# Performance work log

Hardware: AMD Instinct MI355X
Metric: run time of the kernel (lower is better)

Reference implementation:

```python
import jax, jax.numpy as jnp
import numpy as np

B, DIM, H, W = 64, 384, 28, 28
NH, HD, WS, SS = 6, 64, 7, 3
HID = 1536
N = WS * WS
NW = (H // WS) * (W // WS)
SCALE = HD ** -0.25  # qk_scale=None -> head_dim ** -0.25, applied to both q and k
EPS = 1e-5


def _rel_pos_index(ws):
    coords = np.stack(np.meshgrid(np.arange(ws), np.arange(ws), indexing='ij'))  # (2,ws,ws)
    flat = coords.reshape(2, -1)
    rel = (flat[:, :, None] - flat[:, None, :]).transpose(1, 2, 0).copy()  # (N,N,2)
    rel[..., 0] += ws - 1
    rel[..., 1] += ws - 1
    rel[..., 0] *= 2 * ws - 1
    return rel.sum(-1)  # (N,N) int


def _attn_mask(h, w, ws, ss):
    img = np.zeros((h, w))
    cnt = 0
    for hs in (slice(0, -ws), slice(-ws, -ss), slice(-ss, None)):
        for wsl in (slice(0, -ws), slice(-ws, -ss), slice(-ss, None)):
            img[hs, wsl] = cnt
            cnt += 1
    mw = img.reshape(h // ws, ws, w // ws, ws).transpose(0, 2, 1, 3).reshape(-1, ws * ws)  # (nW,N)
    diff = mw[:, None, :] - mw[:, :, None]
    return np.where(diff != 0, -100.0, 0.0).astype(np.float32)  # (nW,N,N)


REL_IDX = jnp.asarray(_rel_pos_index(WS))          # (N,N)
MASK = jnp.asarray(_attn_mask(H, W, WS, SS))       # (NW,N,N)


def _layernorm_bchw(x, w, b):
    mean = jnp.mean(x, axis=1, keepdims=True)
    var = jnp.var(x, axis=1, keepdims=True, ddof=1)  # torch.var_mean is unbiased
    return (x - mean) / jnp.sqrt(var + EPS) * w + b


def setup_inputs() -> dict:
    key = jax.random.key(0)
    ks = jax.random.split(key, 6)
    return {
        'x': jax.random.normal(ks[0], (B, DIM, H, W), jnp.float32),
        'norm1_w': jnp.ones((1, DIM, 1, 1), jnp.float32),
        'norm1_b': jnp.zeros((1, DIM, 1, 1), jnp.float32),
        'qkv_w': jax.random.normal(ks[1], (3 * NH * HD, DIM), jnp.float32) * 0.02,
        'rel_bias_table': jax.random.normal(ks[2], ((2 * WS - 1) ** 2, NH), jnp.float32) * 0.02,
        'proj_w': jax.random.normal(ks[3], (DIM, NH * HD), jnp.float32) * 0.02,
        'norm2_w': jnp.ones((1, DIM, 1, 1), jnp.float32),
        'norm2_b': jnp.zeros((1, DIM, 1, 1), jnp.float32),
        'mlp_w1': jax.random.normal(ks[4], (HID, DIM), jnp.float32) * 0.02,
        'mlp_w3': jax.random.normal(ks[5], (DIM, HID), jnp.float32) * 0.02,
    }


def reference(x, norm1_w, norm1_b, qkv_w, rel_bias_table, proj_w, norm2_w, norm2_b, mlp_w1, mlp_w3):
    b = x.shape[0]
    shortcut = x
    xn = _layernorm_bchw(x, norm1_w, norm1_b)
    xs = jnp.roll(xn, (-SS, -SS), axis=(2, 3))
    # window partition: (B,C,H,W) -> (B*nW, C, WS, WS)
    xw = xs.reshape(b, DIM, H // WS, WS, W // WS, WS).transpose(0, 2, 4, 1, 3, 5).reshape(-1, DIM, WS, WS)
    bw = xw.shape[0]
    # 1x1-conv qkv projection (no bias), then split heads
    qkv = jnp.einsum('oc,bchw->bohw', qkv_w, xw).reshape(bw, 3, NH, HD, N)
    q, k, v = jnp.moveaxis(qkv, 1, 0)  # each (bw, NH, HD, N)
    attn = jnp.einsum('bhdn,bhdm->bhnm', q * SCALE, k * SCALE)  # (bw,NH,N,N)
    bias = rel_bias_table[REL_IDX.reshape(-1)].reshape(N, N, NH).transpose(2, 0, 1)  # (NH,N,N)
    attn = attn + bias[None]
    attn = attn.reshape(b, NW, NH, N, N) + MASK[None, :, None]
    attn = jax.nn.softmax(attn.reshape(bw, NH, N, N), axis=-1)
    out = jnp.einsum('bhnm,bhdm->bhdn', attn, v)  # (bw,NH,HD,N)
    out = out.reshape(bw, NH * HD, WS, WS)
    out = jnp.einsum('oc,bchw->bohw', proj_w, out)
    # window reverse + unshift
    xr = out.reshape(b, H // WS, W // WS, DIM, WS, WS).transpose(0, 3, 1, 4, 2, 5).reshape(b, DIM, H, W)
    xr = jnp.roll(xr, (SS, SS), axis=(2, 3))
    x = shortcut + xr
    # conv MLP (1x1 convs, no bias, exact GELU)
    xn2 = _layernorm_bchw(x, norm2_w, norm2_b)
    h = jax.nn.gelu(jnp.einsum('oc,bchw->bohw', mlp_w1, xn2), approximate=False)
    x = x + jnp.einsum('oc,bchw->bohw', mlp_w3, h)
    return x
```

## Files before the change

kernel.cpp:

```cpp
#include <hip/hip_runtime.h>
#include <hip/hip_bf16.h>


typedef __bf16 bf16x8 __attribute__((ext_vector_type(8)));
typedef __bf16 bf16x4 __attribute__((ext_vector_type(4)));
typedef float  f32x4  __attribute__((ext_vector_type(4)));
typedef float  f32x2  __attribute__((ext_vector_type(2)));
typedef int    i32x4  __attribute__((ext_vector_type(4)));
typedef int    i32x2  __attribute__((ext_vector_type(2)));

#define GAS __attribute__((address_space(1)))
#define LAS __attribute__((address_space(3)))

#if __has_builtin(__builtin_amdgcn_cvt_pk_f32_fp8) && __has_builtin(__builtin_amdgcn_cvt_pk_fp8_f32)
#define HAS_HW_FP8 1
#else
#define HAS_HW_FP8 0
#endif

__device__ __forceinline__ int div7u(int m) { return (m * 37) >> 8; }

#if !HAS_HW_FP8
__device__ __forceinline__ float fp8_dec1(unsigned u) {
  unsigned s = (u >> 7) & 1, e = (u >> 3) & 15, m = u & 7;
  float nrm = __uint_as_float((s << 31) | ((e + 120) << 23) | (m << 20));
  float sub = (s ? -1.f : 1.f) * (float)m * 0.001953125f;
  return e ? nrm : sub;
}
__device__ __forceinline__ unsigned fp8_enc1(float f) {
  f = fminf(fmaxf(f, -448.f), 448.f);
  unsigned u = __float_as_uint(f);
  unsigned s = u >> 31;
  int e8 = (int)((u >> 23) & 255) - 120;
  unsigned m32 = u & 0x7fffff;
  if (e8 <= 0) return s << 7;
  unsigned m = m32 >> 20;
  unsigned rem = m32 & 0xfffff;
  m += (rem > 0x80000u) || (rem == 0x80000u && (m & 1));
  if (m == 8) { m = 0; ++e8; }
  if (e8 > 15 || (e8 == 15 && m == 7)) { e8 = 15; m = 6; }
  return (s << 7) | ((unsigned)e8 << 3) | m;
}
#endif

template <bool HI>
__device__ __forceinline__ f32x2 fp8_cvt2(int w) {
#if HAS_HW_FP8
  return __builtin_amdgcn_cvt_pk_f32_fp8(w, HI);
#else
  unsigned b0 = (w >> (HI ? 16 : 0)) & 255, b1 = (w >> (HI ? 24 : 8)) & 255;
  return (f32x2){fp8_dec1(b0), fp8_dec1(b1)};
#endif
}
template <bool HI>
__device__ __forceinline__ int fp8_pk2(float a, float b, int old) {
#if HAS_HW_FP8
  return __builtin_amdgcn_cvt_pk_fp8_f32(a, b, old, HI);
#else
  unsigned v = fp8_enc1(a) | (fp8_enc1(b) << 8);
  return HI ? (int)(((unsigned)old & 0xffffu) | (v << 16))
            : (int)(((unsigned)old & 0xffff0000u) | v);
#endif
}
__device__ __forceinline__ i32x4 fp8x8_to_bf16x8(i32x2 v) {
  f32x2 a = fp8_cvt2<false>(v[0]), b = fp8_cvt2<true>(v[0]);
  f32x2 c = fp8_cvt2<false>(v[1]), d = fp8_cvt2<true>(v[1]);
  bf16x8 r = {(__bf16)a[0], (__bf16)a[1], (__bf16)b[0], (__bf16)b[1],
              (__bf16)c[0], (__bf16)c[1], (__bf16)d[0], (__bf16)d[1]};
  return __builtin_bit_cast(i32x4, r);
}

__device__ __forceinline__ float gelu_f(float v) {
  float u = v * __builtin_fmaf(0.0356774f, v * v, 0.79788456f);
  float e = __expf(2.f * u);
  float t = 1.f - 2.f * __builtin_amdgcn_rcpf(e + 1.f);
  return 0.5f * v * (1.f + t);
}

__global__ __launch_bounds__(256) void cvt_all_kernel(const float* __restrict__ s0,
                                                      const float* __restrict__ s1,
                                                      const float* __restrict__ s2,
                                                      const float* __restrict__ s3,
                                                      __bf16* __restrict__ d0,
                                                      __bf16* __restrict__ d1,
                                                      __bf16* __restrict__ d2,
                                                      __bf16* __restrict__ d3,
                                                      const float* __restrict__ tbl,
                                                      float* __restrict__ be) {
  int i = blockIdx.x * 256 + threadIdx.x;
  if (i < 442368) { d0[i] = (__bf16)s0[i]; return; }
  i -= 442368;
  if (i < 147456) { d1[i] = (__bf16)s1[i]; return; }
  i -= 147456;
  if (i < 589824) { d2[i] = (__bf16)s2[i]; return; }
  i -= 589824;
  if (i < 589824) { d3[i] = (__bf16)s3[i]; return; }
  i -= 589824;
  if (i < 6 * 64 * 64) {
    int m = i & 63, n = (i >> 6) & 63, h = i >> 12;
    float v = 0.f;
    if (m < 49 && n < 49) {
      int in_ = div7u(n), jn = n - in_ * 7;
      int im  = div7u(m), jm = m - im * 7;
      v = tbl[((in_ - im + 6) * 13 + (jn - jm + 6)) * 6 + h];
    }
    be[i] = v;
  }
}

template <typename TIN>
__global__ __launch_bounds__(256) void ln_t_kernel(const TIN* __restrict__ x,
                                                   const float* __restrict__ gw,
                                                   const float* __restrict__ gb,
                                                   __bf16* __restrict__ out) {
  __shared__ f32x4 ps[16][16], ps2[16][16];
  __shared__ __align__(16) __bf16 tile[64][198];
  const int tid = threadIdx.x;
  const int lane = tid & 63, w = tid >> 6;
  const int gq = lane & 15;
  const int sub = (w << 2) + (lane >> 4);
  const int tok0 = blockIdx.x << 6;
  const int tokg4 = tok0 + (gq << 2);
  const unsigned b = (unsigned)tokg4 / 784u;
  const unsigned p = (unsigned)tokg4 - b * 784u;
  const TIN* xp = x + (size_t)b * 301056u + p;

  f32x4 vals[24];
  f32x4 s4 = {0.f, 0.f, 0.f, 0.f}, s24 = {0.f, 0.f, 0.f, 0.f};
  #pragma unroll
  for (int half = 0; half < 2; ++half)
    #pragma unroll
    for (int k = 0; k < 12; ++k) {
      int c = half * 192 + sub * 12 + k;
      f32x4 v;
      if constexpr (sizeof(TIN) == 4) {
        v = *(const f32x4*)(xp + (size_t)c * 784u);
      } else {
        bf16x4 t = *(const bf16x4*)(xp + (size_t)c * 784u);
        v = (f32x4){(float)t[0], (float)t[1], (float)t[2], (float)t[3]};
      }
      vals[half * 12 + k] = v;
      s4 += v;
      s24 += v * v;
    }
  ps[sub][gq] = s4;
  ps2[sub][gq] = s24;
  __syncthreads();
  f32x4 S = {0.f, 0.f, 0.f, 0.f}, S2 = {0.f, 0.f, 0.f, 0.f};
  #pragma unroll
  for (int i = 0; i < 16; ++i) { S += ps[i][gq]; S2 += ps2[i][gq]; }
  f32x4 mean = S * (1.f / 384.f);
  f32x4 var = (S2 - S * mean) * (1.f / 383.f);
  f32x4 rstd;
  #pragma unroll
  for (int j = 0; j < 4; ++j) rstd[j] = rsqrtf(var[j] + 1e-5f);

  #pragma unroll
  for (int half = 0; half < 2; ++half) {
    if (half) __syncthreads();
    #pragma unroll
    for (int k = 0; k < 12; ++k) {
      int c = half * 192 + sub * 12 + k;
      float wgt = gw[c], bia = gb[c];
      f32x4 v = (vals[half * 12 + k] - mean) * rstd * wgt + bia;
      #pragma unroll
      for (int j = 0; j < 4; ++j)
        tile[(gq << 2) + j][sub * 12 + k] = (__bf16)v[j];
    }
    __syncthreads();
    #pragma unroll
    for (int it = 0; it < 6; ++it) {
      int idx = (it << 8) + tid;
      int row = idx / 24, colc = idx - row * 24;
      bf16x8 vv = *(const bf16x8*)(&tile[row][colc << 3]);
      *(bf16x8*)(out + (size_t)(tok0 + row) * 384 + half * 192 + (colc << 3)) = vv;
    }
  }
}

template <int EPI, int F8>
__global__ __launch_bounds__(256, 3) void gemm_bt(const __bf16* __restrict__ A, int lda,
                                                  const void* __restrict__ BtV, int ldb,
                                                  int K, int My,
                                                  void* __restrict__ outT, int ldo, int ocol,
                                                  void* __restrict__ outR,
                                                  const void* __restrict__ resid,
                                                  int tok_off) {
  constexpr bool B8 = (F8 && EPI >= 2);
  constexpr int esz = B8 ? 1 : 2;
  __shared__ __align__(16) char smem[33792];
  const int tid = threadIdx.x;
  const int lane = tid & 63;
  const int w = tid >> 6;
  const int wr = w >> 1, wc = w & 1;
  const int c = lane & 15, g = lane >> 4;

  const int nwg = gridDim.x;
  const int orig = blockIdx.x;
  const int q = nwg >> 3, r = nwg & 7;
  const int xcd = orig & 7, ii = orig >> 3;
  const int wgid = (xcd < r ? xcd * (q + 1) : r * (q + 1) + (xcd - r) * q) + ii;
  const int bx = wgid / My;
  const int by = wgid - bx * My;
  const int m0 = by << 7;
  const int n0 = bx << 7;

  const __bf16* ap[4];
  const unsigned char* bp[4];
  #pragma unroll
  for (int i = 0; i < 4; ++i) {
    int s = (i << 8) + tid;
    int row = s >> 3;
    int kk = ((s ^ row) & 7) << 3;
    ap[i] = A + (size_t)(m0 + row) * lda + kk;
    bp[i] = (const unsigned char*)BtV + ((size_t)(n0 + row) * ldb + kk) * esz;
  }

  i32x4 sA0, sA1, sA2, sA3;
  i32x4 sB0, sB1, sB2, sB3;
  i32x2 t0, t1, t2, t3;
  auto issue = [&](int k0) {
    sA0 = *(const i32x4*)(ap[0] + k0);
    sA1 = *(const i32x4*)(ap[1] + k0);
    sA2 = *(const i32x4*)(ap[2] + k0);
    sA3 = *(const i32x4*)(ap[3] + k0);
    if constexpr (B8) {
      t0 = *(const i32x2*)(bp[0] + k0);
      t1 = *(const i32x2*)(bp[1] + k0);
      t2 = *(const i32x2*)(bp[2] + k0);
      t3 = *(const i32x2*)(bp[3] + k0);
    } else {
      sB0 = *(const i32x4*)(bp[0] + k0 * 2);
      sB1 = *(const i32x4*)(bp[1] + k0 * 2);
      sB2 = *(const i32x4*)(bp[2] + k0 * 2);
      sB3 = *(const i32x4*)(bp[3] + k0 * 2);
    }
  };
  auto write_lds = [&]() {
    *(i32x4*)(smem +         (((0 << 8) + tid) << 4)) = sA0;
    *(i32x4*)(smem +         (((1 << 8) + tid) << 4)) = sA1;
    *(i32x4*)(smem +         (((2 << 8) + tid) << 4)) = sA2;
    *(i32x4*)(smem +         (((3 << 8) + tid) << 4)) = sA3;
    if constexpr (B8) {
      *(i32x4*)(smem + 16384 + (((0 << 8) + tid) << 4)) = fp8x8_to_bf16x8(t0);
      *(i32x4*)(smem + 16384 + (((1 << 8) + tid) << 4)) = fp8x8_to_bf16x8(t1);
      *(i32x4*)(smem + 16384 + (((2 << 8) + tid) << 4)) = fp8x8_to_bf16x8(t2);
      *(i32x4*)(smem + 16384 + (((3 << 8) + tid) << 4)) = fp8x8_to_bf16x8(t3);
    } else {
      *(i32x4*)(smem + 16384 + (((0 << 8) + tid) << 4)) = sB0;
      *(i32x4*)(smem + 16384 + (((1 << 8) + tid) << 4)) = sB1;
      *(i32x4*)(smem + 16384 + (((2 << 8) + tid) << 4)) = sB2;
      *(i32x4*)(smem + 16384 + (((3 << 8) + tid) << 4)) = sB3;
    }
  };

  f32x4 acc[4][4] = {};
  const int nt = K >> 6;

  issue(0);
  write_lds();
  asm volatile("s_waitcnt lgkmcnt(0)" ::: "memory");
  __builtin_amdgcn_s_barrier();
  __builtin_amdgcn_sched_barrier(0);

  for (int t = 0; t < nt; ++t) {
    if (t + 1 < nt) issue((t + 1) << 6);
    const char* smA = smem;
    const char* smB = smem + 16384;
    #pragma unroll
    for (int ks = 0; ks < 2; ++ks) {
      bf16x8 af[4], bfv[4];
      #pragma unroll
      for (int mi = 0; mi < 4; ++mi) {
        int r2 = (wr << 6) + (mi << 4) + c;
        af[mi] = *(const bf16x8*)(smA + (r2 << 7) + (((ks << 6) + (g << 4)) ^ ((r2 & 7) << 4)));
      }
      #pragma unroll
      for (int nj = 0; nj < 4; ++nj) {
        int r2 = (wc << 6) + (nj << 4) + c;
        bfv[nj] = *(const bf16x8*)(smB + (r2 << 7) + (((ks << 6) + (g << 4)) ^ ((r2 & 7) << 4)));
      }
      #pragma unroll
      for (int mi = 0; mi < 4; ++mi)
        #pragma unroll
        for (int nj = 0; nj < 4; ++nj) {
          if constexpr (EPI >= 2)
            acc[mi][nj] = __builtin_amdgcn_mfma_f32_16x16x32_bf16(bfv[nj], af[mi], acc[mi][nj], 0, 0, 0);
          else
            acc[mi][nj] = __builtin_amdgcn_mfma_f32_16x16x32_bf16(af[mi], bfv[nj], acc[mi][nj], 0, 0, 0);
        }
    }
    __builtin_amdgcn_s_barrier();
    if (t + 1 < nt) {
      write_lds();
      asm volatile("s_waitcnt lgkmcnt(0)" ::: "memory");
    }
    __builtin_amdgcn_s_barrier();
    __builtin_amdgcn_sched_barrier(0);
  }

  if constexpr (EPI <= 1) {
    #pragma unroll
    for (int mi = 0; mi < 4; ++mi)
      #pragma unroll
      for (int nj = 0; nj < 4; ++nj) {
        f32x4 v = acc[mi][nj];
        if constexpr (EPI == 1) {
          #pragma unroll
          for (int r2 = 0; r2 < 4; ++r2) v[r2] = gelu_f(v[r2]);
        }
        bf16x4 pk = {(__bf16)v[0], (__bf16)v[1], (__bf16)v[2], (__bf16)v[3]};
        int nl = (wc << 6) + (nj << 4) + c;
        int ml = (wr << 6) + (mi << 4) + (g << 2);
        *(bf16x4*)(smem + nl * 264 + ml * 2) = pk;
      }
    __syncthreads();
    #pragma unroll
    for (int it = 0; it < 8; ++it) {
      int id = (it << 8) + tid;
      int n = id >> 4, mc = id & 15;
      bf16x8 v = *(const bf16x8*)(smem + n * 264 + (mc << 4));
      if constexpr (F8) {
        int w0 = 0, w1 = 0;
        w0 = fp8_pk2<false>((float)v[0], (float)v[1], w0);
        w0 = fp8_pk2<true>((float)v[2], (float)v[3], w0);
        w1 = fp8_pk2<false>((float)v[4], (float)v[5], w1);
        w1 = fp8_pk2<true>((float)v[6], (float)v[7], w1);
        *(i32x2*)((unsigned char*)outT + (size_t)(n0 + n) * ldo + (ocol + m0 + (mc << 3))) =
            (i32x2){w0, w1};
      } else {
        *(bf16x8*)((__bf16*)outT + (size_t)(n0 + n) * ldo + (ocol + m0 + (mc << 3))) = v;
      }
    }
  } else {
    #pragma unroll
    for (int nj = 0; nj < 4; ++nj) {
      int tokb = tok_off + n0 + (wc << 6) + (nj << 4) + (g << 2);
      unsigned bb = (unsigned)tokb / 784u;
      unsigned pp = (unsigned)tokb - bb * 784u;
      size_t base2 = (size_t)bb * (384u * 784u) + pp;
      #pragma unroll
      for (int mi = 0; mi < 4; ++mi) {
        int o = m0 + (wr << 6) + (mi << 4) + c;
        size_t a2 = base2 + (size_t)o * 784u;
        if constexpr (EPI == 2) {
          bf16x4 rv = *(const bf16x4*)((const __bf16*)resid + a2);
          f32x4 v;
          #pragma unroll
          for (int j = 0; j < 4; ++j) v[j] = acc[mi][nj][j] + (float)rv[j];
          *(f32x4*)((float*)outR + a2) = v;
        } else {
          f32x4 rv = *(const f32x4*)((const float*)resid + a2);
          f32x4 v = acc[mi][nj] + rv;
          bf16x4 pk = {(__bf16)v[0], (__bf16)v[1], (__bf16)v[2], (__bf16)v[3]};
          *(bf16x4*)((__bf16*)outR + a2) = pk;
        }
      }
    }
  }
}

__global__ __launch_bounds__(256, 2) void attn_kernel(const __bf16* __restrict__ qkv,
                                                      const float* __restrict__ be,
                                                      __bf16* __restrict__ outt) {
  __shared__ __align__(16) char smem_all[4][16384];
  const int tid = threadIdx.x;
  const int lane = tid & 63;
  const int w = tid >> 6;
  char* sm = (char*)smem_all[w];
  const int pair = blockIdx.x * 4 + w;
  const int h = pair % 6;
  const int wg = pair / 6;
  const int b = wg >> 4;
  const int wi = wg & 15;
  const int wh = wi >> 2, wwi = wi & 3;
  const int cc = lane & 15, g = lane >> 4;

  {
    int rsub = lane >> 3;
    int slot = lane & 7;
    int dc = (slot ^ rsub) << 3;
    #pragma unroll
    for (int i = 0; i < 8; ++i) {
      int r = i * 8 + rsub;
      int m = r < 49 ? r : 48;
      int im = div7u(m), jm = m - im * 7;
      int sh = wh * 7 + im + 3; if (sh >= 28) sh -= 28;
      int sw = wwi * 7 + jm + 3; if (sw >= 28) sw -= 28;
      size_t trow = (size_t)(b * 784 + sh * 28 + sw) * 1152;
      __builtin_amdgcn_global_load_lds((const GAS void*)(qkv + trow + 384 + h * 64 + dc),
                                       (LAS void*)(sm + i * 1024), 16, 0, 0);
      __builtin_amdgcn_global_load_lds((const GAS void*)(qkv + trow + h * 64 + dc),
                                       (LAS void*)(sm + 8192 + i * 1024), 16, 0, 0);
    }
  }
  asm volatile("s_waitcnt vmcnt(0)" ::: "memory");
  __syncthreads();

  f32x4 sacc[4][4] = {};
  #pragma unroll
  for (int ks = 0; ks < 2; ++ks) {
    bf16x8 kf[4], qf[4];
    #pragma unroll
    for (int mi = 0; mi < 4; ++mi) {
      int r = (mi << 4) + cc;
      kf[mi] = *(const bf16x8*)(sm + (r << 7) + (((ks << 6) + (g << 4)) ^ ((r & 7) << 4)));
    }
    #pragma unroll
    for (int nj = 0; nj < 4; ++nj) {
      int r = (nj << 4) + cc;
      qf[nj] = *(const bf16x8*)(sm + 8192 + (r << 7) + (((ks << 6) + (g << 4)) ^ ((r & 7) << 4)));
    }
    #pragma unroll
    for (int mi = 0; mi < 4; ++mi)
      #pragma unroll
      for (int nj = 0; nj < 4; ++nj)
        sacc[mi][nj] = __builtin_amdgcn_mfma_f32_16x16x32_bf16(kf[mi], qf[nj], sacc[mi][nj], 0, 0, 0);
  }
  __syncthreads();

  int r9m[4][4];
  #pragma unroll
  for (int mi = 0; mi < 4; ++mi)
    #pragma unroll
    for (int rr = 0; rr < 4; ++rr) {
      int m = (mi << 4) + (g << 2) + rr; if (m > 48) m = 48;
      int im = div7u(m), jm = m - im * 7;
      int sh = wh * 7 + im, sw = wwi * 7 + jm;
      r9m[mi][rr] = ((sh < 21) ? 0 : (sh < 25 ? 1 : 2)) * 3 + ((sw < 21) ? 0 : (sw < 25 ? 1 : 2));
    }

  #pragma unroll
  for (int nj = 0; nj < 4; ++nj) {
    int n = (nj << 4) + cc;
    int ncl = n > 48 ? 48 : n;
    int in_ = div7u(ncl), jn = ncl - in_ * 7;
    int shn = wh * 7 + in_, swn = wwi * 7 + jn;
    int r9n = ((shn < 21) ? 0 : (shn < 25 ? 1 : 2)) * 3 + ((swn < 21) ? 0 : (swn < 25 ? 1 : 2));
    float mx = -1e30f;
    #pragma unroll
    for (int mi = 0; mi < 4; ++mi) {
      f32x4 bia = *(const f32x4*)(be + (((h << 6) + n) << 6) + (mi << 4) + (g << 2));
      #pragma unroll
      for (int rr = 0; rr < 4; ++rr) {
        int m = (mi << 4) + (g << 2) + rr;
        float t = (m < 49)
            ? sacc[mi][nj][rr] * 0.125f + bia[rr] + ((r9m[mi][rr] == r9n) ? 0.f : -100.f)
            : -1e30f;
        sacc[mi][nj][rr] = t;
        mx = fmaxf(mx, t);
      }
    }
    mx = fmaxf(mx, __shfl_xor(mx, 16, 64));
    mx = fmaxf(mx, __shfl_xor(mx, 32, 64));
    float sum = 0.f;
    #pragma unroll
    for (int mi = 0; mi < 4; ++mi)
      #pragma unroll
      for (int rr = 0; rr < 4; ++rr) {
        float e = __expf(sacc[mi][nj][rr] - mx);
        sacc[mi][nj][rr] = e;
        sum += e;
      }
    sum += __shfl_xor(sum, 16, 64);
    sum += __shfl_xor(sum, 32, 64);
    float inv = __builtin_amdgcn_rcpf(sum);
    #pragma unroll
    for (int mi = 0; mi < 4; ++mi) {
      bf16x4 pk = {(__bf16)(sacc[mi][nj][0] * inv), (__bf16)(sacc[mi][nj][1] * inv),
                   (__bf16)(sacc[mi][nj][2] * inv), (__bf16)(sacc[mi][nj][3] * inv)};
      *(bf16x4*)(sm + 8192 + (n << 7) + (((mi << 5) + (g << 3)) ^ ((n & 7) << 4))) = pk;
    }
  }

  {
    int ml = lane & 15, dq = lane >> 4;
    #pragma unroll
    for (int it = 0; it < 4; ++it) {
      int m = (it << 4) + ml;
      int mc_ = m > 48 ? 48 : m;
      int im = div7u(mc_), jm = mc_ - im * 7;
      int sh = wh * 7 + im + 3; if (sh >= 28) sh -= 28;
      int sw = wwi * 7 + jm + 3; if (sw >= 28) sw -= 28;
      const __bf16* gv = qkv + (size_t)(b * 784 + sh * 28 + sw) * 1152 + 768 + h * 64;
      #pragma unroll
      for (int hd = 0; hd < 2; ++hd) {
        int dbase = (hd << 5) + (dq << 3);
        bf16x8 v = *(const bf16x8*)(gv + dbase);
        #pragma unroll
        for (int j = 0; j < 8; ++j) {
          int d = dbase + j;
          *(__bf16*)(sm + (d << 7) + ((((m >> 3) ^ (d & 7)) << 4) + ((m & 7) << 1))) = v[j];
        }
      }
    }
  }
  __syncthreads();

  f32x4 oacc[4][4] = {};
  #pragma unroll
  for (int ks = 0; ks < 2; ++ks) {
    bf16x8 pf[4], vf[4];
    #pragma unroll
    for (int ni = 0; ni < 4; ++ni) {
      int n = (ni << 4) + cc;
      pf[ni] = *(const bf16x8*)(sm + 8192 + (n << 7) + (((ks << 6) + (g << 4)) ^ ((n & 7) << 4)));
    }
    #pragma unroll
    for (int dj = 0; dj < 4; ++dj) {
      int d = (dj << 4) + cc;
      vf[dj] = *(const bf16x8*)(sm + (d << 7) + ((((ks << 2) + g) ^ (d & 7)) << 4));
    }
    #pragma unroll
    for (int ni = 0; ni < 4; ++ni)
      #pragma unroll
      for (int dj = 0; dj < 4; ++dj)
        oacc[ni][dj] = __builtin_amdgcn_mfma_f32_16x16x32_bf16(pf[ni], vf[dj], oacc[ni][dj], 0, 0, 0);
  }

  #pragma unroll
  for (int ni = 0; ni < 4; ++ni)
    #pragma unroll
    for (int rr = 0; rr < 4; ++rr) {
      int n = (ni << 4) + (g << 2) + rr;
      if (n < 49) {
        int im = div7u(n), jn = n - im * 7;
        int sh = wh * 7 + im + 3; if (sh >= 28) sh -= 28;
        int sw = wwi * 7 + jn + 3; if (sw >= 28) sw -= 28;
        __bf16* op = outt + (size_t)(b * 784 + sh * 28 + sw) * 384 + h * 64;
        #pragma unroll
        for (int dj = 0; dj < 4; ++dj)
          op[(dj << 4) + cc] = (__bf16)oacc[ni][dj][rr];
      }
    }
}

extern "C" void kernel_launch(void* const* d_in, const int* in_sizes, int n_in,
                              void* d_out, int out_size, void* d_ws, size_t ws_size,
                              hipStream_t stream) {
  (void)in_sizes; (void)n_in; (void)out_size; (void)ws_size;
  const float* x     = (const float*)d_in[0];
  const float* n1w   = (const float*)d_in[1];
  const float* n1b   = (const float*)d_in[2];
  const float* qkvw  = (const float*)d_in[3];
  const float* tbl   = (const float*)d_in[4];
  const float* projw = (const float*)d_in[5];
  const float* n2w   = (const float*)d_in[6];
  const float* n2b   = (const float*)d_in[7];
  const float* w1    = (const float*)d_in[8];
  const float* w3    = (const float*)d_in[9];
  float* out = (float*)d_out;

  char* ws = (char*)d_ws;
  __bf16* bufA = (__bf16*)ws;
  unsigned char* h8 = (unsigned char*)(ws + 38535168);
  __bf16* x2b = (__bf16*)(ws + 38535168 + 77070336);
  float*  be   = (float*)(ws + 154140672);
  __bf16* wq   = (__bf16*)(ws + 154238976);
  __bf16* wp   = wq + 442368;
  __bf16* wm1  = wp + 147456;
  __bf16* wm3  = wm1 + 589824;

  cvt_all_kernel<<<7008, 256, 0, stream>>>(qkvw, projw, w1, w3, wq, wp, wm1, wm3, tbl, be);

  ln_t_kernel<float><<<784, 256, 0, stream>>>(x, n1w, n1b, bufA);
  gemm_bt<0, 0><<<392 * 9, 256, 0, stream>>>(wq, 384, bufA, 384, 384, 9,
                                             (void*)h8, 1152, 0, nullptr, nullptr, 0);
  attn_kernel<<<1536, 256, 0, stream>>>((const __bf16*)h8, be, bufA);
  gemm_bt<3, 0><<<392 * 3, 256, 0, stream>>>(wp, 384, bufA, 384, 384, 3,
                                             nullptr, 0, 0, (void*)x2b, x, 0);
  ln_t_kernel<__bf16><<<784, 256, 0, stream>>>(x2b, n2w, n2b, bufA);
  gemm_bt<1, 1><<<392 * 12, 256, 0, stream>>>(wm1, 384, bufA, 384, 384, 12,
                                              (void*)h8, 1536, 0, nullptr, nullptr, 0);
  gemm_bt<2, 1><<<392 * 3, 256, 0, stream>>>(wm3, 1536, (const void*)h8, 1536, 1536, 3,
                                             nullptr, 0, 0, out, x2b, 0);
}
```

Measured before the change: 344.8 us.

## Run MLP down-projection as native FP8 MFMA GEMM with scaled FP8 weights

Converts the w3 weight to FP8 with a scale of 8 and adds a dedicated gemm_f8 kernel that feeds FP8 operands straight into fp8 MFMA instructions. The old path converted FP8 activations to bf16 in registers before the LDS write. The new path halves the LDS footprint, drops the unpack work and allows higher occupancy. The cost is extra precision loss from quantising the weights to FP8, and the fused residual epilogue is duplicated in a new kernel.

```diff
diff --git a/kernel.cpp b/kernel.cpp
--- a/kernel.cpp
+++ b/kernel.cpp
@@ -5,14 +5,13 @@
 typedef __bf16 bf16x8 __attribute__((ext_vector_type(8)));
 typedef __bf16 bf16x4 __attribute__((ext_vector_type(4)));
 typedef float  f32x4  __attribute__((ext_vector_type(4)));
-typedef float  f32x2  __attribute__((ext_vector_type(2)));
 typedef int    i32x4  __attribute__((ext_vector_type(4)));
 typedef int    i32x2  __attribute__((ext_vector_type(2)));
 
 #define GAS __attribute__((address_space(1)))
 #define LAS __attribute__((address_space(3)))
 
-#if __has_builtin(__builtin_amdgcn_cvt_pk_f32_fp8) && __has_builtin(__builtin_amdgcn_cvt_pk_fp8_f32)
+#if __has_builtin(__builtin_amdgcn_cvt_pk_fp8_f32)
 #define HAS_HW_FP8 1
 #else
 #define HAS_HW_FP8 0
@@ -21,12 +20,6 @@
 __device__ __forceinline__ int div7u(int m) { return (m * 37) >> 8; }
 
 #if !HAS_HW_FP8
-__device__ __forceinline__ float fp8_dec1(unsigned u) {
-  unsigned s = (u >> 7) & 1, e = (u >> 3) & 15, m = u & 7;
-  float nrm = __uint_as_float((s << 31) | ((e + 120) << 23) | (m << 20));
-  float sub = (s ? -1.f : 1.f) * (float)m * 0.001953125f;
-  return e ? nrm : sub;
-}
 __device__ __forceinline__ unsigned fp8_enc1(float f) {
   f = fminf(fmaxf(f, -448.f), 448.f);
   unsigned u = __float_as_uint(f);
@@ -44,15 +37,6 @@
 #endif
 
 template <bool HI>
-__device__ __forceinline__ f32x2 fp8_cvt2(int w) {
-#if HAS_HW_FP8
-  return __builtin_amdgcn_cvt_pk_f32_fp8(w, HI);
-#else
-  unsigned b0 = (w >> (HI ? 16 : 0)) & 255, b1 = (w >> (HI ? 24 : 8)) & 255;
-  return (f32x2){fp8_dec1(b0), fp8_dec1(b1)};
-#endif
-}
-template <bool HI>
 __device__ __forceinline__ int fp8_pk2(float a, float b, int old) {
 #if HAS_HW_FP8
   return __builtin_amdgcn_cvt_pk_fp8_f32(a, b, old, HI);
@@ -62,13 +46,6 @@
             : (int)(((unsigned)old & 0xffff0000u) | v);
 #endif
 }
-__device__ __forceinline__ i32x4 fp8x8_to_bf16x8(i32x2 v) {
-  f32x2 a = fp8_cvt2<false>(v[0]), b = fp8_cvt2<true>(v[0]);
-  f32x2 c = fp8_cvt2<false>(v[1]), d = fp8_cvt2<true>(v[1]);
-  bf16x8 r = {(__bf16)a[0], (__bf16)a[1], (__bf16)b[0], (__bf16)b[1],
-              (__bf16)c[0], (__bf16)c[1], (__bf16)d[0], (__bf16)d[1]};
-  return __builtin_bit_cast(i32x4, r);
-}
 
 __device__ __forceinline__ float gelu_f(float v) {
   float u = v * __builtin_fmaf(0.0356774f, v * v, 0.79788456f);
@@ -84,7 +61,7 @@
                                                       __bf16* __restrict__ d0,
                                                       __bf16* __restrict__ d1,
                                                       __bf16* __restrict__ d2,
-                                                      __bf16* __restrict__ d3,
+                                                      unsigned char* __restrict__ d3,
                                                       const float* __restrict__ tbl,
                                                       float* __restrict__ be) {
   int i = blockIdx.x * 256 + threadIdx.x;
@@ -94,8 +71,13 @@
   i -= 147456;
   if (i < 589824) { d2[i] = (__bf16)s2[i]; return; }
   i -= 589824;
-  if (i < 589824) { d3[i] = (__bf16)s3[i]; return; }
-  i -= 589824;
+  if (i < 294912) {
+    int j = i << 1;
+    int v = fp8_pk2<false>(s3[j] * 8.f, s3[j + 1] * 8.f, 0);
+    ((unsigned short*)d3)[i] = (unsigned short)((unsigned)v & 0xffffu);
+    return;
+  }
+  i -= 294912;
   if (i < 6 * 64 * 64) {
     int m = i & 63, n = (i >> 6) & 63, h = i >> 12;
     float v = 0.f;
@@ -180,14 +162,11 @@
 
 template <int EPI, int F8>
 __global__ __launch_bounds__(256, 3) void gemm_bt(const __bf16* __restrict__ A, int lda,
-                                                  const void* __restrict__ BtV, int ldb,
+                                                  const __bf16* __restrict__ Bt, int ldb,
                                                   int K, int My,
                                                   void* __restrict__ outT, int ldo, int ocol,
                                                   void* __restrict__ outR,
-                                                  const void* __restrict__ resid,
-                                                  int tok_off) {
-  constexpr bool B8 = (F8 && EPI >= 2);
-  constexpr int esz = B8 ? 1 : 2;
+                                                  const float* __restrict__ resid) {
   __shared__ __align__(16) char smem[33792];
   const int tid = threadIdx.x;
   const int lane = tid & 63;
@@ -206,52 +185,36 @@
   const int n0 = bx << 7;
 
   const __bf16* ap[4];
-  const unsigned char* bp[4];
+  const __bf16* bp[4];
   #pragma unroll
   for (int i = 0; i < 4; ++i) {
     int s = (i << 8) + tid;
     int row = s >> 3;
     int kk = ((s ^ row) & 7) << 3;
     ap[i] = A + (size_t)(m0 + row) * lda + kk;
-    bp[i] = (const unsigned char*)BtV + ((size_t)(n0 + row) * ldb + kk) * esz;
-  }
-
-  i32x4 sA0, sA1, sA2, sA3;
-  i32x4 sB0, sB1, sB2, sB3;
-  i32x2 t0, t1, t2, t3;
+    bp[i] = Bt + (size_t)(n0 + row) * ldb + kk;
+  }
+
+  i32x4 sA0, sA1, sA2, sA3, sB0, sB1, sB2, sB3;
   auto issue = [&](int k0) {
     sA0 = *(const i32x4*)(ap[0] + k0);
     sA1 = *(const i32x4*)(ap[1] + k0);
     sA2 = *(const i32x4*)(ap[2] + k0);
     sA3 = *(const i32x4*)(ap[3] + k0);
-    if constexpr (B8) {
-      t0 = *(const i32x2*)(bp[0] + k0);
-      t1 = *(const i32x2*)(bp[1] + k0);
-      t2 = *(const i32x2*)(bp[2] + k0);
-      t3 = *(const i32x2*)(bp[3] + k0);
-    } else {
-      sB0 = *(const i32x4*)(bp[0] + k0 * 2);
-      sB1 = *(const i32x4*)(bp[1] + k0 * 2);
-      sB2 = *(const i32x4*)(bp[2] + k0 * 2);
-      sB3 = *(const i32x4*)(bp[3] + k0 * 2);
-    }
+    sB0 = *(const i32x4*)(bp[0] + k0);
+    sB1 = *(const i32x4*)(bp[1] + k0);
+    sB2 = *(const i32x4*)(bp[2] + k0);
+    sB3 = *(const i32x4*)(bp[3] + k0);
   };
   auto write_lds = [&]() {
     *(i32x4*)(smem +         (((0 << 8) + tid) << 4)) = sA0;
     *(i32x4*)(smem +         (((1 << 8) + tid) << 4)) = sA1;
     *(i32x4*)(smem +         (((2 << 8) + tid) << 4)) = sA2;
     *(i32x4*)(smem +         (((3 << 8) + tid) << 4)) = sA3;
-    if constexpr (B8) {
-      *(i32x4*)(smem + 16384 + (((0 << 8) + tid) << 4)) = fp8x8_to_bf16x8(t0);
-      *(i32x4*)(smem + 16384 + (((1 << 8) + tid) << 4)) = fp8x8_to_bf16x8(t1);
-      *(i32x4*)(smem + 16384 + (((2 << 8) + tid) << 4)) = fp8x8_to_bf16x8(t2);
-      *(i32x4*)(smem + 16384 + (((3 << 8) + tid) << 4)) = fp8x8_to_bf16x8(t3);
-    } else {
-      *(i32x4*)(smem + 16384 + (((0 << 8) + tid) << 4)) = sB0;
-      *(i32x4*)(smem + 16384 + (((1 << 8) + tid) << 4)) = sB1;
-      *(i32x4*)(smem + 16384 + (((2 << 8) + tid) << 4)) = sB2;
-      *(i32x4*)(smem + 16384 + (((3 << 8) + tid) << 4)) = sB3;
-    }
+    *(i32x4*)(smem + 16384 + (((0 << 8) + tid) << 4)) = sB0;
+    *(i32x4*)(smem + 16384 + (((1 << 8) + tid) << 4)) = sB1;
+    *(i32x4*)(smem + 16384 + (((2 << 8) + tid) << 4)) = sB2;
+    *(i32x4*)(smem + 16384 + (((3 << 8) + tid) << 4)) = sB3;
   };
 
   f32x4 acc[4][4] = {};
@@ -284,7 +247,7 @@
       for (int mi = 0; mi < 4; ++mi)
         #pragma unroll
         for (int nj = 0; nj < 4; ++nj) {
-          if constexpr (EPI >= 2)
+          if constexpr (EPI == 3)
             acc[mi][nj] = __builtin_amdgcn_mfma_f32_16x16x32_bf16(bfv[nj], af[mi], acc[mi][nj], 0, 0, 0);
           else
             acc[mi][nj] = __builtin_amdgcn_mfma_f32_16x16x32_bf16(af[mi], bfv[nj], acc[mi][nj], 0, 0, 0);
@@ -335,7 +298,7 @@
   } else {
     #pragma unroll
     for (int nj = 0; nj < 4; ++nj) {
-      int tokb = tok_off + n0 + (wc << 6) + (nj << 4) + (g << 2);
+      int tokb = n0 + (wc << 6) + (nj << 4) + (g << 2);
       unsigned bb = (unsigned)tokb / 784u;
       unsigned pp = (unsigned)tokb - bb * 784u;
       size_t base2 = (size_t)bb * (384u * 784u) + pp;
@@ -343,19 +306,119 @@
       for (int mi = 0; mi < 4; ++mi) {
         int o = m0 + (wr << 6) + (mi << 4) + c;
         size_t a2 = base2 + (size_t)o * 784u;
-        if constexpr (EPI == 2) {
-          bf16x4 rv = *(const bf16x4*)((const __bf16*)resid + a2);
-          f32x4 v;
-          #pragma unroll
-          for (int j = 0; j < 4; ++j) v[j] = acc[mi][nj][j] + (float)rv[j];
-          *(f32x4*)((float*)outR + a2) = v;
-        } else {
-          f32x4 rv = *(const f32x4*)((const float*)resid + a2);
-          f32x4 v = acc[mi][nj] + rv;
-          bf16x4 pk = {(__bf16)v[0], (__bf16)v[1], (__bf16)v[2], (__bf16)v[3]};
-          *(bf16x4*)((__bf16*)outR + a2) = pk;
-        }
-      }
+        f32x4 rv = *(const f32x4*)(resid + a2);
+        f32x4 v = acc[mi][nj] + rv;
+        bf16x4 pk = {(__bf16)v[0], (__bf16)v[1], (__bf16)v[2], (__bf16)v[3]};
+        *(bf16x4*)((__bf16*)outR + a2) = pk;
+      }
+    }
+  }
+}
+
+__global__ __launch_bounds__(256, 4) void gemm_f8(const unsigned char* __restrict__ A,
+                                                  const unsigned char* __restrict__ Bt,
+                                                  int My,
+                                                  float* __restrict__ outR,
+                                                  const __bf16* __restrict__ resid) {
+  __shared__ __align__(16) char smem[16384];
+  const int tid = threadIdx.x;
+  const int lane = tid & 63;
+  const int w = tid >> 6;
+  const int wr = w >> 1, wc = w & 1;
+  const int c = lane & 15, g = lane >> 4;
+
+  const int nwg = gridDim.x;
+  const int orig = blockIdx.x;
+  const int q = nwg >> 3, r = nwg & 7;
+  const int xcd = orig & 7, ii = orig >> 3;
+  const int wgid = (xcd < r ? xcd * (q + 1) : r * (q + 1) + (xcd - r) * q) + ii;
+  const int bx = wgid / My;
+  const int by = wgid - bx * My;
+  const int m0 = by << 7;
+  const int n0 = bx << 7;
+
+  const unsigned char* ap[4];
+  const unsigned char* bp[4];
+  #pragma unroll
+  for (int i = 0; i < 4; ++i) {
+    int s = (i << 8) + tid;
+    int row = s >> 3;
+    int off = ((s ^ row) & 7) << 3;
+    ap[i] = A + (size_t)(m0 + row) * 1536 + off;
+    bp[i] = Bt + (size_t)(n0 + row) * 1536 + off;
+  }
+
+  i32x2 a0, a1, a2r, a3, b0, b1, b2, b3;
+  auto issue = [&](int k0) {
+    a0 = *(const i32x2*)(ap[0] + k0); b0 = *(const i32x2*)(bp[0] + k0);
+    a1 = *(const i32x2*)(ap[1] + k0); b1 = *(const i32x2*)(bp[1] + k0);
+    a2r = *(const i32x2*)(ap[2] + k0); b2 = *(const i32x2*)(bp[2] + k0);
+    a3 = *(const i32x2*)(ap[3] + k0); b3 = *(const i32x2*)(bp[3] + k0);
+  };
+  auto write_lds = [&]() {
+    *(i32x2*)(smem +        (((0 << 8) + tid) << 3)) = a0;
+    *(i32x2*)(smem +        (((1 << 8) + tid) << 3)) = a1;
+    *(i32x2*)(smem +        (((2 << 8) + tid) << 3)) = a2r;
+    *(i32x2*)(smem +        (((3 << 8) + tid) << 3)) = a3;
+    *(i32x2*)(smem + 8192 + (((0 << 8) + tid) << 3)) = b0;
+    *(i32x2*)(smem + 8192 + (((1 << 8) + tid) << 3)) = b1;
+    *(i32x2*)(smem + 8192 + (((2 << 8) + tid) << 3)) = b2;
+    *(i32x2*)(smem + 8192 + (((3 << 8) + tid) << 3)) = b3;
+  };
+
+  f32x4 acc[4][4] = {};
+
+  issue(0);
+  write_lds();
+  asm volatile("s_waitcnt lgkmcnt(0)" ::: "memory");
+  __builtin_amdgcn_s_barrier();
+  __builtin_amdgcn_sched_barrier(0);
+
+  for (int t = 0; t < 24; ++t) {
+    if (t + 1 < 24) issue((t + 1) << 6);
+    #pragma unroll
+    for (int ks = 0; ks < 2; ++ks) {
+      long af[4], bfv[4];
+      #pragma unroll
+      for (int mi = 0; mi < 4; ++mi) {
+        int r2 = (wr << 6) + (mi << 4) + c;
+        af[mi] = *(const long*)(smem + (r2 << 6) + ((((ks << 2) + g) ^ (r2 & 7)) << 3));
+      }
+      #pragma unroll
+      for (int nj = 0; nj < 4; ++nj) {
+        int r2 = (wc << 6) + (nj << 4) + c;
+        bfv[nj] = *(const long*)(smem + 8192 + (r2 << 6) + ((((ks << 2) + g) ^ (r2 & 7)) << 3));
+      }
+      #pragma unroll
+      for (int mi = 0; mi < 4; ++mi)
+        #pragma unroll
+        for (int nj = 0; nj < 4; ++nj)
+          acc[mi][nj] = __builtin_amdgcn_mfma_f32_16x16x32_fp8_fp8(bfv[nj], af[mi], acc[mi][nj], 0, 0, 0);
+    }
+    __builtin_amdgcn_s_barrier();
+    if (t + 1 < 24) {
+      write_lds();
+      asm volatile("s_waitcnt lgkmcnt(0)" ::: "memory");
+    }
+    __builtin_amdgcn_s_barrier();
+    __builtin_amdgcn_sched_barrier(0);
+  }
+
+  #pragma unroll
+  for (int nj = 0; nj < 4; ++nj) {
+    int tokb = n0 + (wc << 6) + (nj << 4) + (g << 2);
+    unsigned bb = (unsigned)tokb / 784u;
+    unsigned pp = (unsigned)tokb - bb * 784u;
+    size_t base2 = (size_t)bb * (384u * 784u) + pp;
+    #pragma unroll
+    for (int mi = 0; mi < 4; ++mi) {
+      int o = m0 + (wr << 6) + (mi << 4) + c;
+      size_t a2 = base2 + (size_t)o * 784u;
+      bf16x4 rv = *(const bf16x4*)(resid + a2);
+      f32x4 v;
+      #pragma unroll
+      for (int j = 0; j < 4; ++j) v[j] = __builtin_fmaf(acc[mi][nj][j], 0.125f, (float)rv[j]);
+      *(f32x4*)(outR + a2) = v;
     }
   }
 }
@@ -559,19 +622,18 @@
   __bf16* wq   = (__bf16*)(ws + 154238976);
   __bf16* wp   = wq + 442368;
   __bf16* wm1  = wp + 147456;
-  __bf16* wm3  = wm1 + 589824;
-
-  cvt_all_kernel<<<7008, 256, 0, stream>>>(qkvw, projw, w1, w3, wq, wp, wm1, wm3, tbl, be);
+  unsigned char* w3f8 = (unsigned char*)(wm1 + 589824);
+
+  cvt_all_kernel<<<5856, 256, 0, stream>>>(qkvw, projw, w1, w3, wq, wp, wm1, w3f8, tbl, be);
 
   ln_t_kernel<float><<<784, 256, 0, stream>>>(x, n1w, n1b, bufA);
   gemm_bt<0, 0><<<392 * 9, 256, 0, stream>>>(wq, 384, bufA, 384, 384, 9,
-                                             (void*)h8, 1152, 0, nullptr, nullptr, 0);
+                                             (void*)h8, 1152, 0, nullptr, nullptr);
   attn_kernel<<<1536, 256, 0, stream>>>((const __bf16*)h8, be, bufA);
   gemm_bt<3, 0><<<392 * 3, 256, 0, stream>>>(wp, 384, bufA, 384, 384, 3,
-                                             nullptr, 0, 0, (void*)x2b, x, 0);
+                                             nullptr, 0, 0, (void*)x2b, x);
   ln_t_kernel<__bf16><<<784, 256, 0, stream>>>(x2b, n2w, n2b, bufA);
   gemm_bt<1, 1><<<392 * 12, 256, 0, stream>>>(wm1, 384, bufA, 384, 384, 12,
-                                              (void*)h8, 1536, 0, nullptr, nullptr, 0);
-  gemm_bt<2, 1><<<392 * 3, 256, 0, stream>>>(wm3, 1536, (const void*)h8, 1536, 1536, 3,
-                                             nullptr, 0, 0, out, x2b, 0);
-}
+                                              (void*)h8, 1536, 0, nullptr, nullptr);
+  gemm_f8<<<392 * 3, 256, 0, stream>>>(w3f8, h8, 3, out, x2b);
+}
```

Measured after the change: 340.4 us. About the same (-1.3%).
